# Kernel optimization log

Hardware: AMD Instinct MI355X
Metric: run time of the kernel (lower is better)

## Reference

```python
import jax, jax.numpy as jnp
import numpy as np

N, n, D1, D2 = 16, 1024, 64, 64


def setup_inputs() -> dict:
    key = jax.random.key(0)
    ks = jax.random.split(key, 17)
    f = lambda k, shape: jax.random.normal(k, shape, dtype=jnp.float32)
    return {
        "A": f(ks[0], (N, n, n)),
        "X": f(ks[1], (N, n, D1)),
        "coeffs": f(ks[2], (5,)),
        "wA1": f(ks[3], (1, D1)),
        "wA2": f(ks[4], (1, D1)),
        "w11": f(ks[5], (D2, D1)),
        "w12": f(ks[6], (D2, D1)),
        "w13": f(ks[7], (D2, 1)),
        "w14": f(ks[8], (D2, 1)),
        "w15": f(ks[9], (D2, 1)),
        "w16": f(ks[10], (D2, 1)),
        "w21": f(ks[11], (D2, D1)),
        "w22": f(ks[12], (D2, D1)),
        "w23": f(ks[13], (D2, 1)),
        "w24": f(ks[14], (D2, 1)),
        "w25": f(ks[15], (D2, 1)),
        "w26": f(ks[16], (D2, 1)),
    }


def reference(A, X, coeffs, wA1, wA2, w11, w12, w13, w14, w15, w16,
              w21, w22, w23, w24, w25, w26):
    nn_ = A.shape[-1]
    diag = jnp.diagonal(A, axis1=-2, axis2=-1)          # (N, n)
    mean_diag = diag.mean(-1)                            # (N,)
    rowmean = A.mean(-1)                                 # (N, n) mean over columns
    mean_all = rowmean.mean(-1)                          # (N,)
    mean_X = X.mean(1)                                   # (N, D1)

    p1 = X @ wA1[0]                                      # (N, n)   Linear(D1->1) per node
    p2 = mean_X @ wA2[0]                                 # (N,)     Linear(D1->1) on mean

    # adjacency transform: scalar-weighted A + scalar stats + symmetrized row stats
    A_t = (coeffs[0] * A
           + (coeffs[1] * mean_all + coeffs[2] * mean_diag + p2)[:, None, None]
           + coeffs[3] * (rowmean[:, None, :] + rowmean[:, :, None])
           + coeffs[4] * (diag[:, None, :] + diag[:, :, None])
           + p1[:, None, :] + p1[:, :, None])             # (N, n, n)

    def node_transform(w_x, w_mx, w_col, w_diag, w_mdiag, w_mall):
        per_graph = (mean_X @ w_mx.T                      # (N, D2)
                     + mean_diag[:, None] * w_mdiag[:, 0][None, :]
                     + mean_all[:, None] * w_mall[:, 0][None, :])
        return (jnp.einsum('bnd,ed->bne', X, w_x)         # (N, n, D2)
                + rowmean[:, :, None] * w_col[:, 0]
                + diag[:, :, None] * w_diag[:, 0]
                + per_graph[:, None, :])

    X1_t = node_transform(w11, w12, w13, w14, w15, w16)
    X2_t = node_transform(w21, w22, w23, w24, w25, w26)

    out = A_t @ X2_t / nn_ + X1_t                         # (N, n, D2)
    return (A_t, out)
```

## Files before the change

### kernel.cpp

```cpp
#include <hip/hip_runtime.h>
#include <hip/hip_bf16.h>

#define NGRAPH 16
#define NNODE 1024
#define DDIM 64

typedef __attribute__((ext_vector_type(8))) short bf16x8;
typedef __attribute__((ext_vector_type(4))) float f32x4;

#define OFF_ROWSUM 0
#define OFF_DIAG   16384
#define OFF_P1     32768
#define OFF_R      49152
#define OFF_CS     65536
#define OFF_S      73728
#define OFF_S2P    75840
#define OFF_R2P    92224
#define OFF_BASE0  110656
#define OFF_X2T    1159232

__device__ __forceinline__ unsigned short f2bf(float f) {
    unsigned int u = __float_as_uint(f);
    u = (u + 0x7fffu + ((u >> 16) & 1u)) >> 16;
    return (unsigned short)u;
}

__device__ __forceinline__ unsigned int cvt_pk_bf16(float lo, float hi) {
    unsigned int r;
    asm("v_cvt_pk_bf16_f32 %0, %1, %2" : "=v"(r) : "v"(lo), "v"(hi));
    return r;
}

__device__ __forceinline__ float wave_reduce(float v) {
    #pragma unroll
    for (int off = 32; off; off >>= 1) v += __shfl_down(v, off, 64);
    return v;
}

__global__ __launch_bounds__(256) void kA_stats(const float* __restrict__ A,
                                                const float* __restrict__ X,
                                                const float* __restrict__ wA1,
                                                float* __restrict__ rowsum,
                                                float* __restrict__ diagv,
                                                float* __restrict__ p1,
                                                float* __restrict__ colsum_part) {
    if (blockIdx.x < NGRAPH * NNODE / 4) {
        int row  = blockIdx.x * 4 + (threadIdx.x >> 6);
        int lane = threadIdx.x & 63;
        const float4* b4 = (const float4*)(A + (size_t)row * NNODE);
        float sum = 0.f;
        #pragma unroll
        for (int it = 0; it < 4; ++it) {
            float4 v = b4[lane + it * 64];
            sum += v.x + v.y + v.z + v.w;
        }
        sum = wave_reduce(sum);
        if (lane == 0) {
            rowsum[row] = sum;
            int i = row & (NNODE - 1);
            diagv[row] = ((const float*)b4)[i];
        }
    } else {
        int bid  = blockIdx.x - NGRAPH * NNODE / 4;
        int b    = bid >> 3;
        int blk  = bid & 7;
        int wv   = threadIdx.x >> 6;
        int lane = threadIdx.x & 63;
        float w = wA1[lane];
        float cs = 0.f;
        int row0 = blk * 128 + wv * 32;
        const float* Xb = X + (size_t)b * NNODE * DDIM;
        for (int rI = 0; rI < 32; ++rI) {
            int i = row0 + rI;
            float x = Xb[i * DDIM + lane];
            cs += x;
            float v = wave_reduce(x * w);
            if (lane == 0) p1[b * NNODE + i] = v;
        }
        __shared__ float csl[4][64];
        csl[wv][lane] = cs;
        __syncthreads();
        if (threadIdx.x < 64) {
            float t = csl[0][lane] + csl[1][lane] + csl[2][lane] + csl[3][lane];
            colsum_part[(b * 8 + blk) * 64 + lane] = t;
        }
    }
}

__global__ __launch_bounds__(256) void kB_nodes(const float* __restrict__ X,
                                                const float* __restrict__ coeffs,
                                                const float* __restrict__ wA2,
                                                const float* __restrict__ w11,
                                                const float* __restrict__ w12,
                                                const float* __restrict__ w13,
                                                const float* __restrict__ w14,
                                                const float* __restrict__ w15,
                                                const float* __restrict__ w16,
                                                const float* __restrict__ w21,
                                                const float* __restrict__ w22,
                                                const float* __restrict__ w23,
                                                const float* __restrict__ w24,
                                                const float* __restrict__ w25,
                                                const float* __restrict__ w26,
                                                const float* __restrict__ rowsum,
                                                const float* __restrict__ diagv,
                                                const float* __restrict__ colsum_part,
                                                const float* __restrict__ p1g,
                                                float* __restrict__ rws,
                                                float* __restrict__ base0,
                                                unsigned short* __restrict__ x2tg,
                                                float* __restrict__ S2part,
                                                float* __restrict__ R2part,
                                                float* __restrict__ sArr) {
    __shared__ float Xl[64][68];
    __shared__ float w1l[64][68];
    __shared__ float w2l[64][68];
    __shared__ unsigned short X2Tl[64][68];
    __shared__ float rm_l[64], dg_l[64], r_l[64];
    __shared__ float redS[4][64], redR[4][64];
    __shared__ float redA[4], redD[4];
    __shared__ float mxs[64], p2s;
    __shared__ float pg1_l[64], pg2_l[64];

    int b    = blockIdx.x >> 4;
    int tile = blockIdx.x & 15;
    int i0   = tile * 64;
    int tid  = threadIdx.x;
    int e    = tid & 63;
    int wv   = tid >> 6;

    const float* Xg = X + (size_t)b * (NNODE * DDIM) + (size_t)i0 * DDIM;
    #pragma unroll
    for (int it = 0; it < 4; ++it) {
        int g   = it * 256 + tid;
        int row = g >> 4;
        int c4  = (g & 15) << 2;
        float4 v  = ((const float4*)Xg)[g];
        *(float4*)&Xl[row][c4] = v;
        float4 v1 = ((const float4*)w11)[g];
        *(float4*)&w1l[row][c4] = v1;
        float4 v2 = ((const float4*)w21)[g];
        *(float4*)&w2l[row][c4] = v2;
    }

    float sa = 0.f, sd = 0.f;
    for (int i = tid; i < NNODE; i += 256) {
        sa += rowsum[b * NNODE + i];
        sd += diagv[b * NNODE + i];
    }
    sa = wave_reduce(sa); sd = wave_reduce(sd);
    if (e == 0) { redA[wv] = sa; redD[wv] = sd; }
    if (tid < 64) {
        float mx = 0.f;
        for (int k = 0; k < 8; ++k) mx += colsum_part[(b * 8 + k) * 64 + tid];
        mxs[tid] = mx * (1.f / (float)NNODE);
    }
    __syncthreads();
    float mean_all  = (redA[0] + redA[1] + redA[2] + redA[3]) * (1.f / ((float)NNODE * (float)NNODE));
    float mean_diag = (redD[0] + redD[1] + redD[2] + redD[3]) * (1.f / (float)NNODE);
    float c3 = coeffs[3], c4c = coeffs[4];

    if (wv == 0) {
        float a1 = 0.f;
        for (int d = 0; d < 64; ++d) a1 += mxs[d] * w12[e * 64 + d];
        pg1_l[e] = a1 + mean_diag * w15[e] + mean_all * w16[e];
    } else if (wv == 1) {
        float a2 = 0.f;
        for (int d = 0; d < 64; ++d) a2 += mxs[d] * w22[e * 64 + d];
        pg2_l[e] = a2 + mean_diag * w25[e] + mean_all * w26[e];
    } else if (wv == 2) {
        float v = wave_reduce(mxs[e] * wA2[e]);
        if (e == 0) p2s = v;
    } else {
        float rs  = rowsum[b * NNODE + i0 + e];
        float dgv = diagv[b * NNODE + i0 + e];
        float rmv = rs * (1.f / (float)NNODE);
        rm_l[e] = rmv;
        dg_l[e] = dgv;
        float rv = c3 * rmv + c4c * dgv + p1g[b * NNODE + i0 + e];
        r_l[e] = rv;
        rws[b * NNODE + i0 + e] = rv;
    }
    __syncthreads();
    if (tile == 0 && tid == 0)
        sArr[b] = coeffs[1] * mean_all + coeffs[2] * mean_diag + p2s;

    float w13e = w13[e], w14e = w14[e], w23e = w23[e], w24e = w24[e];
    float pg1e = pg1_l[e], pg2e = pg2_l[e];

    float acc1[16], acc2[16];
    #pragma unroll
    for (int t = 0; t < 16; ++t) { acc1[t] = 0.f; acc2[t] = 0.f; }

    for (int d0 = 0; d0 < 64; d0 += 4) {
        float4 w1v = *(const float4*)&w1l[e][d0];
        float4 w2v = *(const float4*)&w2l[e][d0];
        #pragma unroll
        for (int t = 0; t < 16; ++t) {
            int li = wv + 4 * t;
            float4 xv = *(const float4*)&Xl[li][d0];
            acc1[t] += xv.x * w1v.x + xv.y * w1v.y + xv.z * w1v.z + xv.w * w1v.w;
            acc2[t] += xv.x * w2v.x + xv.y * w2v.y + xv.z * w2v.z + xv.w * w2v.w;
        }
    }

    float s2acc = 0.f, r2acc = 0.f;
    #pragma unroll
    for (int t = 0; t < 16; ++t) {
        int li = wv + 4 * t;
        int i  = i0 + li;
        float rmv = rm_l[li], dgv = dg_l[li];
        float x2t = acc2[t] + rmv * w23e + dgv * w24e + pg2e;
        float b0  = acc1[t] + rmv * w13e + dgv * w14e + pg1e;
        base0[((size_t)(b * NNODE + i)) * 64 + e] = b0;
        X2Tl[e][li] = f2bf(x2t);
        s2acc += x2t;
        r2acc += r_l[li] * x2t;
    }
    redS[wv][e] = s2acc;
    redR[wv][e] = r2acc;
    __syncthreads();

    for (int k = 0; k < 16; ++k) {
        int ep = wv * 16 + k;
        unsigned short v = X2Tl[ep][e];
        x2tg[((size_t)(b * 64 + ep)) * NNODE + i0 + e] = v;
    }
    if (tid < 64) {
        float s2 = redS[0][tid] + redS[1][tid] + redS[2][tid] + redS[3][tid];
        float r2 = redR[0][tid] + redR[1][tid] + redR[2][tid] + redR[3][tid];
        S2part[(b * 16 + tile) * 64 + tid] = s2;
        R2part[(b * 16 + tile) * 64 + tid] = r2;
    }
}

__global__ __launch_bounds__(256) void kC_main(const float* __restrict__ A,
                                               const float* __restrict__ coeffs,
                                               const float* __restrict__ sArr,
                                               const float* __restrict__ rArr,
                                               const unsigned short* __restrict__ x2tg,
                                               const float* __restrict__ base0,
                                               const float* __restrict__ S2part,
                                               const float* __restrict__ R2part,
                                               float* __restrict__ At,
                                               float* __restrict__ outp) {
    __shared__ float r_lds[1024];
    __shared__ float s2_lds[64], r2_lds[64];

    int b    = blockIdx.x >> 4;
    int tb   = blockIdx.x & 15;
    int tid  = threadIdx.x;
    int lane = tid & 63, wv = tid >> 6;
    int i0   = (tb * 4 + wv) * 16;
    int m    = lane & 15, q = lane >> 4;

    float4 rv = ((const float4*)(rArr + b * NNODE))[tid];
    *(float4*)&r_lds[tid * 4] = rv;
    if (tid < 64) {
        float s2 = 0.f, r2 = 0.f;
        #pragma unroll
        for (int t = 0; t < 16; ++t) {
            s2 += S2part[(b * 16 + t) * 64 + tid];
            r2 += R2part[(b * 16 + t) * 64 + tid];
        }
        s2_lds[tid] = s2 * (1.f / (float)NNODE);
        r2_lds[tid] = r2 * (1.f / (float)NNODE);
    }

    float sb  = sArr[b];
    float c0  = coeffs[0];
    float c0n = c0 * (1.f / (float)NNODE);

    const float* Aw  = A  + ((size_t)(b * NNODE + i0 + m)) * NNODE + q * 8;
    float*       Atw = At + ((size_t)(b * NNODE + i0 + m)) * NNODE + q * 8;
    const unsigned short* Bw = x2tg + ((size_t)(b * 64 + m)) * NNODE + q * 8;

    f32x4 a[8], an[8];
    #pragma unroll
    for (int ks = 0; ks < 4; ++ks) {
        a[2 * ks]     = *(const f32x4*)(Aw + ks * 32);
        a[2 * ks + 1] = *(const f32x4*)(Aw + ks * 32 + 4);
    }

    f32x4 acc[4];
    #pragma unroll
    for (int s = 0; s < 4; ++s) acc[s] = (f32x4){0.f, 0.f, 0.f, 0.f};

    __syncthreads();

    float bse = sb + r_lds[i0 + m];

    #pragma unroll 2
    for (int kt = 0; kt < 8; ++kt) {
        bf16x8 Bf[4][4];
        #pragma unroll
        for (int s = 0; s < 4; ++s) {
            #pragma unroll
            for (int ks = 0; ks < 4; ++ks) {
                Bf[s][ks] = *(const bf16x8*)(Bw + (size_t)s * 16 * NNODE + kt * 128 + ks * 32);
            }
        }

        if (kt < 7) {
            #pragma unroll
            for (int ks = 0; ks < 4; ++ks) {
                an[2 * ks]     = *(const f32x4*)(Aw + (kt + 1) * 128 + ks * 32);
                an[2 * ks + 1] = *(const f32x4*)(Aw + (kt + 1) * 128 + ks * 32 + 4);
            }
        }

        bf16x8 pka[4];
        #pragma unroll
        for (int ks = 0; ks < 4; ++ks) {
            int cb = kt * 128 + ks * 32 + q * 8;
            f32x4 rj0 = *(const f32x4*)&r_lds[cb];
            f32x4 rj1 = *(const f32x4*)&r_lds[cb + 4];
            f32x4 ac0 = a[2 * ks], ac1 = a[2 * ks + 1];
            f32x4 t0, t1;
            t0.x = fmaf(c0, ac0.x, bse + rj0.x);
            t0.y = fmaf(c0, ac0.y, bse + rj0.y);
            t0.z = fmaf(c0, ac0.z, bse + rj0.z);
            t0.w = fmaf(c0, ac0.w, bse + rj0.w);
            t1.x = fmaf(c0, ac1.x, bse + rj1.x);
            t1.y = fmaf(c0, ac1.y, bse + rj1.y);
            t1.z = fmaf(c0, ac1.z, bse + rj1.z);
            t1.w = fmaf(c0, ac1.w, bse + rj1.w);
            *(f32x4*)(Atw + kt * 128 + ks * 32)     = t0;
            *(f32x4*)(Atw + kt * 128 + ks * 32 + 4) = t1;

            union { uint4 u; bf16x8 h; } cv;
            cv.u.x = cvt_pk_bf16(ac0.x, ac0.y);
            cv.u.y = cvt_pk_bf16(ac0.z, ac0.w);
            cv.u.z = cvt_pk_bf16(ac1.x, ac1.y);
            cv.u.w = cvt_pk_bf16(ac1.z, ac1.w);
            pka[ks] = cv.h;
        }

        #pragma unroll
        for (int s = 0; s < 4; ++s) {
            #pragma unroll
            for (int ks = 0; ks < 4; ++ks) {
                acc[s] = __builtin_amdgcn_mfma_f32_16x16x32_bf16(pka[ks], Bf[s][ks], acc[s], 0, 0, 0);
            }
        }

        if (kt < 7) {
            #pragma unroll
            for (int u = 0; u < 8; ++u) a[u] = an[u];
        }
    }

    #pragma unroll
    for (int s = 0; s < 4; ++s) {
        float s2 = s2_lds[s * 16 + m];
        float r2 = r2_lds[s * 16 + m];
        #pragma unroll
        for (int reg = 0; reg < 4; ++reg) {
            int i = i0 + q * 4 + reg;
            float v = acc[s][reg] * c0n
                    + base0[((size_t)(b * NNODE + i)) * 64 + s * 16 + m]
                    + (sb + r_lds[i]) * s2 + r2;
            outp[((size_t)(b * NNODE + i)) * 64 + s * 16 + m] = v;
        }
    }
}

extern "C" void kernel_launch(void* const* d_in, const int* in_sizes, int n_in,
                              void* d_out, int out_size, void* d_ws, size_t ws_size,
                              hipStream_t stream) {
    const float* A      = (const float*)d_in[0];
    const float* X      = (const float*)d_in[1];
    const float* coeffs = (const float*)d_in[2];
    const float* wA1    = (const float*)d_in[3];
    const float* wA2    = (const float*)d_in[4];
    const float* w11    = (const float*)d_in[5];
    const float* w12    = (const float*)d_in[6];
    const float* w13    = (const float*)d_in[7];
    const float* w14    = (const float*)d_in[8];
    const float* w15    = (const float*)d_in[9];
    const float* w16    = (const float*)d_in[10];
    const float* w21    = (const float*)d_in[11];
    const float* w22    = (const float*)d_in[12];
    const float* w23    = (const float*)d_in[13];
    const float* w24    = (const float*)d_in[14];
    const float* w25    = (const float*)d_in[15];
    const float* w26    = (const float*)d_in[16];

    float* ws  = (float*)d_ws;
    float* At  = (float*)d_out;
    float* out = (float*)d_out + (size_t)NGRAPH * NNODE * NNODE;

    float* rowsum = ws + OFF_ROWSUM;
    float* diagv  = ws + OFF_DIAG;
    float* p1     = ws + OFF_P1;
    float* rws    = ws + OFF_R;
    float* cspart = ws + OFF_CS;
    float* sArr   = ws + OFF_S;
    float* S2part = ws + OFF_S2P;
    float* R2part = ws + OFF_R2P;
    float* base0  = ws + OFF_BASE0;
    unsigned short* x2tg = (unsigned short*)(ws + OFF_X2T);

    kA_stats<<<NGRAPH * NNODE / 4 + NGRAPH * 8, 256, 0, stream>>>(
        A, X, wA1, rowsum, diagv, p1, cspart);
    kB_nodes<<<NGRAPH * 16, 256, 0, stream>>>(
        X, coeffs, wA2, w11, w12, w13, w14, w15, w16,
        w21, w22, w23, w24, w25, w26,
        rowsum, diagv, cspart, p1,
        rws, base0, x2tg, S2part, R2part, sArr);
    kC_main<<<NGRAPH * 16, 256, 0, stream>>>(
        A, coeffs, sArr, rws, x2tg, base0, S2part, R2part, At, out);
}
```

Measured before the change: 203.6 us.

## Split K dimension of main kernel across wave pairs and double grid

Each 16-row tile in the main fused kernel is now processed by two waves, each covering half of the column range. The partial MFMA accumulators are exchanged and summed through shared memory before the epilogue. The grid doubles so more waves are in flight to hide the latency of streaming A. The cost is an extra LDS reduction and a barrier, plus an occupancy hint in the launch bounds.

```diff
diff --git a/kernel.cpp b/kernel.cpp
--- a/kernel.cpp
+++ b/kernel.cpp
@@ -234,7 +234,7 @@
     }
 }
 
-__global__ __launch_bounds__(256) void kC_main(const float* __restrict__ A,
+__global__ __launch_bounds__(256, 2) void kC_main(const float* __restrict__ A,
                                                const float* __restrict__ coeffs,
                                                const float* __restrict__ sArr,
                                                const float* __restrict__ rArr,
@@ -246,12 +246,16 @@
                                                float* __restrict__ outp) {
     __shared__ float r_lds[1024];
     __shared__ float s2_lds[64], r2_lds[64];
-
-    int b    = blockIdx.x >> 4;
-    int tb   = blockIdx.x & 15;
+    __shared__ float accx[2][2][64][8];
+
+    int b    = blockIdx.x >> 5;
+    int tb   = blockIdx.x & 31;
     int tid  = threadIdx.x;
     int lane = tid & 63, wv = tid >> 6;
-    int i0   = (tb * 4 + wv) * 16;
+    int tIdx = wv >> 1;
+    int h    = wv & 1;
+    int tile = tb * 2 + tIdx;
+    int i0   = tile * 16;
     int m    = lane & 15, q = lane >> 4;
 
     float4 rv = ((const float4*)(rArr + b * NNODE))[tid];
@@ -275,11 +279,13 @@
     float*       Atw = At + ((size_t)(b * NNODE + i0 + m)) * NNODE + q * 8;
     const unsigned short* Bw = x2tg + ((size_t)(b * 64 + m)) * NNODE + q * 8;
 
+    int kt0 = 4 * h;
+
     f32x4 a[8], an[8];
     #pragma unroll
     for (int ks = 0; ks < 4; ++ks) {
-        a[2 * ks]     = *(const f32x4*)(Aw + ks * 32);
-        a[2 * ks + 1] = *(const f32x4*)(Aw + ks * 32 + 4);
+        a[2 * ks]     = *(const f32x4*)(Aw + kt0 * 128 + ks * 32);
+        a[2 * ks + 1] = *(const f32x4*)(Aw + kt0 * 128 + ks * 32 + 4);
     }
 
     f32x4 acc[4];
@@ -290,8 +296,10 @@
 
     float bse = sb + r_lds[i0 + m];
 
-    #pragma unroll 2
-    for (int kt = 0; kt < 8; ++kt) {
+    #pragma unroll
+    for (int j = 0; j < 4; ++j) {
+        int kt = kt0 + j;
+
         bf16x8 Bf[4][4];
         #pragma unroll
         for (int s = 0; s < 4; ++s) {
@@ -301,7 +309,7 @@
             }
         }
 
-        if (kt < 7) {
+        if (j < 3) {
             #pragma unroll
             for (int ks = 0; ks < 4; ++ks) {
                 an[2 * ks]     = *(const f32x4*)(Aw + (kt + 1) * 128 + ks * 32);
@@ -328,12 +336,12 @@
             *(f32x4*)(Atw + kt * 128 + ks * 32)     = t0;
             *(f32x4*)(Atw + kt * 128 + ks * 32 + 4) = t1;
 
-            union { uint4 u; bf16x8 h; } cv;
+            union { uint4 u; bf16x8 hh; } cv;
             cv.u.x = cvt_pk_bf16(ac0.x, ac0.y);
             cv.u.y = cvt_pk_bf16(ac0.z, ac0.w);
             cv.u.z = cvt_pk_bf16(ac1.x, ac1.y);
             cv.u.w = cvt_pk_bf16(ac1.z, ac1.w);
-            pka[ks] = cv.h;
+            pka[ks] = cv.hh;
         }
 
         #pragma unroll
@@ -344,20 +352,29 @@
             }
         }
 
-        if (kt < 7) {
+        if (j < 3) {
             #pragma unroll
             for (int u = 0; u < 8; ++u) a[u] = an[u];
         }
     }
 
     #pragma unroll
-    for (int s = 0; s < 4; ++s) {
+    for (int j = 0; j < 2; ++j) {
+        int s = 2 * (1 - h) + j;
+        *(f32x4*)&accx[tIdx][h][lane][4 * j] = acc[s];
+    }
+    __syncthreads();
+
+    #pragma unroll
+    for (int j = 0; j < 2; ++j) {
+        int s = 2 * h + j;
+        f32x4 part = *(const f32x4*)&accx[tIdx][1 - h][lane][4 * j];
         float s2 = s2_lds[s * 16 + m];
         float r2 = r2_lds[s * 16 + m];
         #pragma unroll
         for (int reg = 0; reg < 4; ++reg) {
             int i = i0 + q * 4 + reg;
-            float v = acc[s][reg] * c0n
+            float v = (acc[s][reg] + part[reg]) * c0n
                     + base0[((size_t)(b * NNODE + i)) * 64 + s * 16 + m]
                     + (sb + r_lds[i]) * s2 + r2;
             outp[((size_t)(b * NNODE + i)) * 64 + s * 16 + m] = v;
@@ -408,6 +425,6 @@
         w21, w22, w23, w24, w25, w26,
         rowsum, diagv, cspart, p1,
         rws, base0, x2tg, S2part, R2part, sArr);
-    kC_main<<<NGRAPH * 16, 256, 0, stream>>>(
+    kC_main<<<NGRAPH * 32, 256, 0, stream>>>(
         A, coeffs, sArr, rws, x2tg, base0, S2part, R2part, At, out);
 }
```

New measurement: 210.4 us. 1.03x slower.
